# Kernel tuning notes

Measured on AMD Instinct MI355X. Metric: run time of the kernel, lower is better.

## Reference

```python
import jax, jax.numpy as jnp
import numpy as np

B, S, D, H, DH = 4, 2048, 1024, 16, 64
INIT_STD = 0.02
IGNORE = -100000.0


def setup_inputs() -> dict:
    key = jax.random.key(0)
    ks = jax.random.split(key, 5)
    x = jax.random.normal(ks[0], (B, S, D), dtype=jnp.float32)
    W_Q = INIT_STD * jax.random.normal(ks[1], (H, D, DH), dtype=jnp.float32)
    W_K = INIT_STD * jax.random.normal(ks[2], (H, D, DH), dtype=jnp.float32)
    W_V = INIT_STD * jax.random.normal(ks[3], (H, D, DH), dtype=jnp.float32)
    W_O = INIT_STD * jax.random.normal(ks[4], (H, DH, D), dtype=jnp.float32)
    b_Q = jnp.zeros((H, DH), dtype=jnp.float32)
    b_K = jnp.zeros((H, DH), dtype=jnp.float32)
    b_V = jnp.zeros((H, DH), dtype=jnp.float32)
    b_O = jnp.zeros((D,), dtype=jnp.float32)
    return {"x": x, "W_Q": W_Q, "b_Q": b_Q, "W_K": W_K, "b_K": b_K,
            "W_V": W_V, "b_V": b_V, "W_O": W_O, "b_O": b_O}


def reference(x, W_Q, b_Q, W_K, b_K, W_V, b_V, W_O, b_O):
    # x: (B, S, D); projections -> (B, S, H, DH)
    Q = jnp.einsum('bqd,hde->bqhe', x, W_Q) + b_Q
    K = jnp.einsum('bkd,hde->bkhe', x, W_K) + b_K
    V = jnp.einsum('bkd,hde->bkhe', x, W_V) + b_V
    d_head = Q.shape[-1]
    # scores: (B, H, Sq, Sk)
    scores = jnp.einsum('bqhe,bkhe->bhqk', Q, K) / np.sqrt(d_head).astype(np.float32)
    s = scores.shape[-1]
    causal = jnp.triu(jnp.ones((s, s), dtype=bool), k=1)
    scores = jnp.where(causal, jnp.float32(IGNORE), scores)
    A = jax.nn.softmax(scores, axis=-1)
    z = jnp.einsum('bhqk,bkhe->bqhe', A, V)
    # output projection: sum over heads + bias
    attn_out = jnp.einsum('bqhe,hed->bqd', z, W_O) + b_O
    return attn_out
```

## Files before the change

kernel.cpp:

```cpp
#include <hip/hip_runtime.h>


#define B_ 4
#define S_ 2048
#define D_ 1024
#define H_ 16
#define DH_ 64

typedef unsigned short ushort_t;
typedef __attribute__((ext_vector_type(4))) short short4v;
typedef __attribute__((ext_vector_type(8))) short short8v;
typedef __attribute__((ext_vector_type(4))) float floatx4;
typedef __attribute__((ext_vector_type(4))) unsigned short ushort4v;

static __device__ __forceinline__ ushort_t f2bf(float f) {
    union { float f; unsigned u; } v; v.f = f;
    unsigned r = v.u + 0x7fffu + ((v.u >> 16) & 1u);
    return (ushort_t)(r >> 16);
}

static __device__ __forceinline__ float fast_exp2(float x) {
#if __has_builtin(__builtin_amdgcn_exp2f)
    return __builtin_amdgcn_exp2f(x);
#else
    return exp2f(x);
#endif
}

static __device__ __forceinline__ unsigned pack_bf16_tr(float lo, float hi) {
    union { float f; unsigned u; } a, b;
    a.f = lo; b.f = hi;
    return __builtin_amdgcn_perm(b.u, a.u, 0x07060302u);
}

static __device__ __forceinline__ void g2lds16(const void* g, void* l) {
    __builtin_amdgcn_global_load_lds(
        (__attribute__((address_space(1))) void*)(unsigned long long)(size_t)g,
        (__attribute__((address_space(3))) void*)(unsigned int)(size_t)l,
        16, 0, 0);
}

__global__ void prep_kernel(const float* __restrict__ x,
                            const float* __restrict__ wq, const float* __restrict__ wk,
                            const float* __restrict__ wv, const float* __restrict__ wo,
                            ushort_t* __restrict__ xb, ushort_t* __restrict__ wt,
                            ushort_t* __restrict__ wot) {
    __shared__ float tile[32][33];
    int bid = blockIdx.x;
    int tid = threadIdx.x;
    if (bid < 8192) {
        int i = (bid * 256 + tid) * 4;
        float4 v = *(const float4*)&x[i];
        ushort4v o;
        o[0] = f2bf(v.x); o[1] = f2bf(v.y); o[2] = f2bf(v.z); o[3] = f2bf(v.w);
        *(ushort4v*)&xb[i] = o;
        return;
    }
    const float* src;
    ushort_t* d;
    int C, r0, c0;
    if (bid < 11264) {
        int t = bid - 8192;
        int z = t / 64, r = t % 64;
        src = (z < 16 ? wq : (z < 32 ? wk : wv)) + (size_t)(z & 15) * 65536;
        d = wt + (size_t)z * 65536;
        C = 64; r0 = (r >> 1) * 32; c0 = (r & 1) * 32;
    } else {
        int t = bid - 11264;
        int z = t / 64, r = t % 64;
        src = wo + (size_t)z * 65536;
        d = wot + (size_t)z * 64;
        C = 1024; r0 = (r & 1) * 32; c0 = (r >> 1) * 32;
    }
    int tx = tid & 31, ty = tid >> 5;
#pragma unroll
    for (int i = 0; i < 4; ++i)
        tile[ty + i * 8][tx] = src[(size_t)(r0 + ty + i * 8) * C + c0 + tx];
    __syncthreads();
#pragma unroll
    for (int i = 0; i < 4; ++i)
        d[(size_t)(c0 + ty + i * 8) * 1024 + r0 + tx] = f2bf(tile[tx][ty + i * 8]);
}


#define GQ_BAR() __builtin_amdgcn_s_barrier()
#define GQ_VM4 do { asm volatile("s_waitcnt vmcnt(4)"); __builtin_amdgcn_sched_barrier(0); } while (0)
#define GQ_VM2 do { asm volatile("s_waitcnt vmcnt(2)"); __builtin_amdgcn_sched_barrier(0); } while (0)
#define GQ_VM0 do { asm volatile("s_waitcnt vmcnt(0)"); __builtin_amdgcn_sched_barrier(0); } while (0)
#define GQ_WAITLG do { asm volatile("s_waitcnt lgkmcnt(0)"); __builtin_amdgcn_sched_barrier(0); } while (0)

#define GQ_READS_B(KB)                                                          \
    _Pragma("unroll") for (int nt = 0; nt < 4; ++nt)                            \
        bfr[KB][nt] = *(const short8v*)&cB[(wn * 64 + nt * 16) * 64 + ((KB) ? kb1 : kb0)];

#define GQ_READS_A(MH, KB)                                                      \
    _Pragma("unroll") for (int i = 0; i < 4; ++i)                               \
        af[i] = *(const short8v*)&cA[(wm * 128 + ((MH) * 4 + i) * 16) * 64 + ((KB) ? kb1 : kb0)];

#define GQ_MFMA(MH, KB)                                                         \
    GQ_WAITLG;                                                                  \
    __builtin_amdgcn_s_setprio(1);                                              \
    _Pragma("unroll") for (int i = 0; i < 4; ++i)                               \
        _Pragma("unroll") for (int nt = 0; nt < 4; ++nt)                        \
            acc[(MH) * 4 + i][nt] = __builtin_amdgcn_mfma_f32_16x16x32_bf16(    \
                af[i], bfr[KB][nt], acc[(MH) * 4 + i][nt], 0, 0, 0);            \
    __builtin_amdgcn_s_setprio(0);                                              \
    __builtin_amdgcn_sched_barrier(0);

#define GQ_KSTEP(CA, CB, S1, S2, S3, S4, WMID, WEND) do {                       \
    const ushort_t* cA = (CA); const ushort_t* cB = (CB);                       \
    short8v af[4]; short8v bfr[2][4];                                           \
    GQ_READS_B(0) GQ_READS_A(0, 0) S1; GQ_BAR();                                \
    GQ_MFMA(0, 0) GQ_BAR();                                                     \
    GQ_READS_B(1) GQ_READS_A(0, 1) S2; GQ_BAR();                                \
    GQ_MFMA(0, 1) WMID; GQ_BAR();                                               \
    GQ_READS_A(1, 0) S3; GQ_BAR();                                              \
    GQ_MFMA(1, 0) GQ_BAR();                                                     \
    GQ_READS_A(1, 1) S4; GQ_BAR();                                              \
    GQ_MFMA(1, 1) WEND; GQ_BAR();                                               \
} while (0)

__global__ __launch_bounds__(512, 2) void gemm_qkv(const ushort_t* __restrict__ A,
                                                   const ushort_t* __restrict__ Wt,
                                                   const float* __restrict__ bq,
                                                   const float* __restrict__ bk,
                                                   const float* __restrict__ bv,
                                                   ushort_t* __restrict__ Qw,
                                                   ushort_t* __restrict__ Kw,
                                                   ushort_t* __restrict__ Vw) {
    __shared__ ushort_t sA[2][256 * 64];
    __shared__ ushort_t sB[2][256 * 64];
    const int tid = threadIdx.x;
    const int lane = tid & 63, w = tid >> 6;
    const int lq = lane & 15, quad = lane >> 4;
    const int wm = w >> 2, wn = w & 3;
    const int m0 = blockIdx.x * 256, n0 = blockIdx.y * 256;

    const int kb0 = lq * 64 + ((quad ^ (lq & 7)) << 3);
    const int kb1 = lq * 64 + (((4 | quad) ^ (lq & 7)) << 3);

    const int uR = ((w & 4) << 5) + (w & 3) * 16;

    auto stageA2 = [&](ushort_t* dst, int kk, int R0) __attribute__((always_inline)) {
#pragma unroll
        for (int j = 0; j < 2; ++j) {
            int rr = R0 + j * 8 + (lane >> 3);
            int cc = (lane & 7) ^ (rr & 7);
            g2lds16(&A[(size_t)(m0 + rr) * 1024 + kk + cc * 8], &dst[(R0 + j * 8) * 64]);
        }
    };
    auto stageB2 = [&](ushort_t* dst, int kk, int R0) __attribute__((always_inline)) {
#pragma unroll
        for (int j = 0; j < 2; ++j) {
            int rr = R0 + j * 8 + (lane >> 3);
            int cc = (lane & 7) ^ (rr & 7);
            g2lds16(&Wt[(size_t)(n0 + rr) * 1024 + kk + cc * 8], &dst[(R0 + j * 8) * 64]);
        }
    };

    floatx4 acc[8][4] = {};

    stageA2(sA[0], 0, uR);
    stageB2(sB[0], 0, w * 32);
    stageB2(sB[0], 0, w * 32 + 16);
    stageA2(sA[0], 0, uR + 64);
    GQ_VM2;
    GQ_BAR();

    int p = 0;
    for (int t = 0; t < 15; ++t) {
        const int kk = (t + 1) * 64;
        ushort_t* nA = sA[p ^ 1];
        ushort_t* nB = sB[p ^ 1];
        GQ_KSTEP(sA[p], sB[p],
                 stageA2(nA, kk, uR),
                 stageB2(nB, kk, w * 32),
                 stageB2(nB, kk, w * 32 + 16),
                 stageA2(nA, kk, uR + 64),
                 GQ_VM4, GQ_VM2);
        p ^= 1;
    }
    GQ_KSTEP(sA[1], sB[1], (void)0, (void)0, (void)0, (void)0, GQ_VM0, (void)0);

    const int mat = blockIdx.y >> 2;
    const float* bias = mat == 0 ? bq : (mat == 1 ? bk : bv);
    const int colbase = (blockIdx.y & 3) * 256 + wn * 64;
    float bias_v[4];
#pragma unroll
    for (int nt = 0; nt < 4; ++nt) bias_v[nt] = bias[colbase + nt * 16 + lq];

#pragma unroll
    for (int mt = 0; mt < 8; ++mt) {
#pragma unroll
        for (int nt = 0; nt < 4; ++nt) {
            int row0 = m0 + wm * 128 + mt * 16 + quad * 4;
            int col = colbase + nt * 16 + lq;
            int h = col >> 6, e = col & 63;
            if (mat == 2) {
                int b = row0 >> 11, s = row0 & 2047;
                ushort4v pk;
#pragma unroll
                for (int rg = 0; rg < 4; ++rg) pk[rg] = f2bf(acc[mt][nt][rg] + bias_v[nt]);
                *(ushort4v*)&Vw[((size_t)((b << 4) | h) * 64 + e) * 2048 + s] = pk;
            } else {
                ushort_t* Du = mat == 0 ? Qw : Kw;
#pragma unroll
                for (int rg = 0; rg < 4; ++rg) {
                    int row = row0 + rg;
                    int b = row >> 11, s = row & 2047;
                    float v = acc[mt][nt][rg] + bias_v[nt];
                    if (mat == 0) v *= 0.18033688011112042f;
                    Du[((size_t)((b << 4) | h) * 2048 + s) * 64 + e] = f2bf(v);
                }
            }
        }
    }
}

#define VROW 140
__global__ __launch_bounds__(256) void attn_kernel(const ushort_t* __restrict__ Q,
                                                   const ushort_t* __restrict__ Kg,
                                                   const ushort_t* __restrict__ Vt,
                                                   ushort_t* __restrict__ Z) {
    __shared__ ushort_t sK[2][128 * 64];
    __shared__ ushort_t sV[64 * VROW];
    const int tid = threadIdx.x;
    const int lane = tid & 63, w = tid >> 6;
    const int lq = lane & 15, quad = lane >> 4;
    const int bh = blockIdx.x;
    const int b = bh >> 4, h = bh & 15;
    const ushort_t* Qp = Q + (size_t)bh * S_ * DH_;
    const ushort_t* Kp = Kg + (size_t)bh * S_ * DH_;
    const ushort_t* Vp = Vt + (size_t)bh * DH_ * S_;

    const int kbase0 = lq * 64 + ((quad ^ (lq & 7)) << 3);
    const int kbase1 = lq * 64 + (((4 | quad) ^ (lq & 7)) << 3);
    const int vbase = lq * VROW + quad * 4;
    const int vr = w * 16 + (lane >> 2);
    const int vc = (lane & 3) * 32;

    const floatx4 fzero = {0.f, 0.f, 0.f, 0.f};

    auto stageK = [&](int kt, int bs) __attribute__((always_inline)) {
        ushort_t* dK = sK[bs];
#pragma unroll
        for (int p = 0; p < 4; ++p) {
            int rrk = w * 32 + p * 8 + (lane >> 3);
            int ck = (lane & 7) ^ (rrk & 7);
            g2lds16(&Kp[(size_t)(kt * 128 + rrk) * 64 + ck * 8], &dK[(w * 32 + p * 8) * 64]);
        }
    };
    auto loadV = [&](int kt, short8v* vr4) __attribute__((always_inline)) {
        const ushort_t* src = &Vp[(size_t)vr * 2048 + kt * 128 + vc];
#pragma unroll
        for (int j = 0; j < 4; ++j) vr4[j] = *(const short8v*)&src[j * 8];
    };
    auto writeV = [&](const short8v* vr4) __attribute__((always_inline)) {
        ushort_t* dst = &sV[vr * VROW + vc];
#pragma unroll
        for (int j = 0; j < 4; ++j) *(short8v*)&dst[j * 8] = vr4[j];
    };

    for (int pass = 0; pass < 2; ++pass) {
        const int qt = pass == 0 ? (int)blockIdx.y : 15 - (int)blockIdx.y;
        const int q0 = qt * 128;

        short8v qf[2][2];
#pragma unroll
        for (int qi = 0; qi < 2; ++qi)
#pragma unroll
            for (int ks = 0; ks < 2; ++ks)
                qf[qi][ks] = *(const short8v*)&Qp[(size_t)(q0 + w * 32 + qi * 16 + lq) * DH_ + ks * 32 + quad * 8];

        float l_i[2] = {0.f, 0.f};
        floatx4 o[2][4] = {};
        short8v vreg[4];

        stageK(0, 0);
        loadV(0, vreg);

        for (int kt = 0; kt <= qt; ++kt) {
            const bool diag = (kt == qt);
            const ushort_t* cK = sK[kt & 1];

            __syncthreads();
            writeV(vreg);
            if (kt < qt) {
                stageK(kt + 1, (kt + 1) & 1);
                loadV(kt + 1, vreg);
            }

            floatx4 st[8][2];
#pragma unroll
            for (int si = 0; si < 8; ++si) {
                short8v a0 = *(const short8v*)&cK[kbase0 + si * 1024];
                short8v a1 = *(const short8v*)&cK[kbase1 + si * 1024];
#pragma unroll
                for (int qi = 0; qi < 2; ++qi) {
                    st[si][qi] = __builtin_amdgcn_mfma_f32_16x16x32_bf16(a0, qf[qi][0], fzero, 0, 0, 0);
                    st[si][qi] = __builtin_amdgcn_mfma_f32_16x16x32_bf16(a1, qf[qi][1], st[si][qi], 0, 0, 0);
                }
            }

            short4v pf[8][2];
#pragma unroll
            for (int qi = 0; qi < 2; ++qi) {
                const int qg = q0 + w * 32 + qi * 16 + lq;
                float lsum = 0.f;
#pragma unroll
                for (int si = 0; si < 8; ++si) {
                    float p[4];
#pragma unroll
                    for (int rg = 0; rg < 4; ++rg) {
                        float v = st[si][qi][rg];
                        if (diag) {
                            int sg = kt * 128 + si * 16 + quad * 4 + rg;
                            if (sg > qg) v = -1e30f;
                        }
                        p[rg] = fast_exp2(v);
                        lsum += p[rg];
                    }
                    union { unsigned u[2]; short4v v4; } pk;
                    pk.u[0] = pack_bf16_tr(p[0], p[1]);
                    pk.u[1] = pack_bf16_tr(p[2], p[3]);
                    pf[si][qi] = pk.v4;
                }
                l_i[qi] += lsum;
            }

            __syncthreads();

#pragma unroll
            for (int ksp = 0; ksp < 8; ++ksp) {
#pragma unroll
                for (int et = 0; et < 4; ++et) {
                    short4v vf = *(const short4v*)&sV[vbase + et * (16 * VROW) + ksp * 16];
#pragma unroll
                    for (int qi = 0; qi < 2; ++qi)
                        o[qi][et] = __builtin_amdgcn_mfma_f32_16x16x16bf16_1k(pf[ksp][qi], vf, o[qi][et], 0, 0, 0);
                }
            }
        }

#pragma unroll
        for (int qi = 0; qi < 2; ++qi) {
            float lf = l_i[qi];
            lf += __shfl_xor(lf, 16);
            lf += __shfl_xor(lf, 32);
            float linv[4];
#pragma unroll
            for (int rg = 0; rg < 4; ++rg) linv[rg] = 1.0f / __shfl(lf, quad * 4 + rg);
#pragma unroll
            for (int et = 0; et < 4; ++et) {
#pragma unroll
                for (int rg = 0; rg < 4; ++rg) {
                    int qg = q0 + w * 32 + qi * 16 + quad * 4 + rg;
                    int e = et * 16 + lq;
                    Z[((size_t)(b * S_ + qg) * H_ + h) * DH_ + e] = f2bf(o[qi][et][rg] * linv[rg]);
                }
            }
        }
    }
}

__global__ __launch_bounds__(256) void gemm_o(const ushort_t* __restrict__ A,
                                              const ushort_t* __restrict__ Bt,
                                              const float* __restrict__ bias,
                                              float* __restrict__ Dst) {
    __shared__ ushort_t sA[128 * 64];
    __shared__ ushort_t sB[128 * 64];
    const int tid = threadIdx.x;
    const int lane = tid & 63, w = tid >> 6;
    const int lq = lane & 15, quad = lane >> 4;
    const int wm = w >> 1, wn = w & 1;
    const int m0 = blockIdx.x * 128, n0 = blockIdx.y * 128;

    floatx4 acc[4][4] = {};

    for (int k0 = 0; k0 < 1024; k0 += 64) {
        __syncthreads();
#pragma unroll
        for (int p = 0; p < 4; ++p) {
            int rr = w * 32 + p * 8 + (lane >> 3);
            int cc = (lane & 7) ^ (rr & 7);
            g2lds16(&A[(size_t)(m0 + rr) * 1024 + k0 + cc * 8], &sA[(w * 32 + p * 8) * 64]);
            g2lds16(&Bt[(size_t)(n0 + rr) * 1024 + k0 + cc * 8], &sB[(w * 32 + p * 8) * 64]);
        }
        __syncthreads();
#pragma unroll
        for (int ks = 0; ks < 2; ++ks) {
            short8v af[4], bfr[4];
#pragma unroll
            for (int t = 0; t < 4; ++t) {
                int ma = wm * 64 + t * 16 + lq;
                af[t] = *(const short8v*)&sA[ma * 64 + ((((ks << 2) | quad) ^ (ma & 7)) << 3)];
                int nb = wn * 64 + t * 16 + lq;
                bfr[t] = *(const short8v*)&sB[nb * 64 + ((((ks << 2) | quad) ^ (nb & 7)) << 3)];
            }
#pragma unroll
            for (int mt = 0; mt < 4; ++mt)
#pragma unroll
                for (int nt = 0; nt < 4; ++nt)
                    acc[mt][nt] = __builtin_amdgcn_mfma_f32_16x16x32_bf16(af[mt], bfr[nt], acc[mt][nt], 0, 0, 0);
        }
    }

    float bias_v[4];
#pragma unroll
    for (int nt = 0; nt < 4; ++nt) bias_v[nt] = bias[n0 + wn * 64 + nt * 16 + lq];

#pragma unroll
    for (int mt = 0; mt < 4; ++mt) {
#pragma unroll
        for (int nt = 0; nt < 4; ++nt) {
            int row0 = m0 + wm * 64 + mt * 16 + quad * 4;
            int col = n0 + wn * 64 + nt * 16 + lq;
#pragma unroll
            for (int rg = 0; rg < 4; ++rg)
                Dst[(size_t)(row0 + rg) * 1024 + col] = acc[mt][nt][rg] + bias_v[nt];
        }
    }
}

extern "C" void kernel_launch(void* const* d_in, const int* in_sizes, int n_in,
                              void* d_out, int out_size, void* d_ws, size_t ws_size,
                              hipStream_t stream) {
    const float* x  = (const float*)d_in[0];
    const float* wq = (const float*)d_in[1];
    const float* bq = (const float*)d_in[2];
    const float* wk = (const float*)d_in[3];
    const float* bk = (const float*)d_in[4];
    const float* wv = (const float*)d_in[5];
    const float* bv = (const float*)d_in[6];
    const float* wo = (const float*)d_in[7];
    const float* bo = (const float*)d_in[8];

    char* ws = (char*)d_ws;
    size_t off = 0;
    ushort_t* xb  = (ushort_t*)(ws + off); off += (size_t)8192 * 1024 * 2;
    ushort_t* wt  = (ushort_t*)(ws + off); off += (size_t)3 * 1024 * 1024 * 2;
    ushort_t* wot = (ushort_t*)(ws + off); off += (size_t)1024 * 1024 * 2;
    ushort_t* Qw  = (ushort_t*)(ws + off); off += (size_t)8192 * 1024 * 2;
    ushort_t* Kw  = (ushort_t*)(ws + off); off += (size_t)8192 * 1024 * 2;
    ushort_t* Vw  = (ushort_t*)(ws + off); off += (size_t)8192 * 1024 * 2;
    ushort_t* Zw  = (ushort_t*)(ws + off); off += (size_t)8192 * 1024 * 2;

    prep_kernel<<<12288, 256, 0, stream>>>(x, wq, wk, wv, wo, xb, wt, wot);
    gemm_qkv<<<dim3(32, 12), 512, 0, stream>>>(xb, wt, bq, bk, bv, Qw, Kw, Vw);
    attn_kernel<<<dim3(64, 8), 256, 0, stream>>>(Qw, Kw, Vw, Zw);
    gemm_o<<<dim3(64, 8), 256, 0, stream>>>(Zw, wot, bo, (float*)d_out);
}
```

Baseline: 254.8 us.

## Shrink QKV GEMM tile to 128 rows and raise MFMA priority in attention

The QKV projection GEMM now uses a 128x256 output tile instead of 256x256, which doubles the grid to 768 blocks and halves the A-tile shared memory and accumulator registers. The load staging, wait counts and epilogue row mapping are reworked to fit. The aim is better fill of the GPU's many compute units with more, smaller blocks, at the cost of more B-matrix reloads per output. The attention kernel also wraps its QK and PV MFMA loops in s_setprio to favour the matrix-issuing waves.

Measured after the change: 262.6 us. +3.1%, slower.

```diff
diff --git a/kernel.cpp b/kernel.cpp
--- a/kernel.cpp
+++ b/kernel.cpp
@@ -85,7 +85,7 @@
 
 #define GQ_BAR() __builtin_amdgcn_s_barrier()
 #define GQ_VM4 do { asm volatile("s_waitcnt vmcnt(4)"); __builtin_amdgcn_sched_barrier(0); } while (0)
-#define GQ_VM2 do { asm volatile("s_waitcnt vmcnt(2)"); __builtin_amdgcn_sched_barrier(0); } while (0)
+#define GQ_VM1 do { asm volatile("s_waitcnt vmcnt(1)"); __builtin_amdgcn_sched_barrier(0); } while (0)
 #define GQ_VM0 do { asm volatile("s_waitcnt vmcnt(0)"); __builtin_amdgcn_sched_barrier(0); } while (0)
 #define GQ_WAITLG do { asm volatile("s_waitcnt lgkmcnt(0)"); __builtin_amdgcn_sched_barrier(0); } while (0)
 
@@ -94,22 +94,22 @@
         bfr[KB][nt] = *(const short8v*)&cB[(wn * 64 + nt * 16) * 64 + ((KB) ? kb1 : kb0)];
 
 #define GQ_READS_A(MH, KB)                                                      \
-    _Pragma("unroll") for (int i = 0; i < 4; ++i)                               \
-        af[i] = *(const short8v*)&cA[(wm * 128 + ((MH) * 4 + i) * 16) * 64 + ((KB) ? kb1 : kb0)];
+    _Pragma("unroll") for (int i = 0; i < 2; ++i)                               \
+        af[i] = *(const short8v*)&cA[(wm * 64 + ((MH) * 2 + i) * 16) * 64 + ((KB) ? kb1 : kb0)];
 
 #define GQ_MFMA(MH, KB)                                                         \
     GQ_WAITLG;                                                                  \
     __builtin_amdgcn_s_setprio(1);                                              \
-    _Pragma("unroll") for (int i = 0; i < 4; ++i)                               \
+    _Pragma("unroll") for (int i = 0; i < 2; ++i)                               \
         _Pragma("unroll") for (int nt = 0; nt < 4; ++nt)                        \
-            acc[(MH) * 4 + i][nt] = __builtin_amdgcn_mfma_f32_16x16x32_bf16(    \
-                af[i], bfr[KB][nt], acc[(MH) * 4 + i][nt], 0, 0, 0);            \
+            acc[(MH) * 2 + i][nt] = __builtin_amdgcn_mfma_f32_16x16x32_bf16(    \
+                af[i], bfr[KB][nt], acc[(MH) * 2 + i][nt], 0, 0, 0);            \
     __builtin_amdgcn_s_setprio(0);                                              \
     __builtin_amdgcn_sched_barrier(0);
 
 #define GQ_KSTEP(CA, CB, S1, S2, S3, S4, WMID, WEND) do {                       \
     const ushort_t* cA = (CA); const ushort_t* cB = (CB);                       \
-    short8v af[4]; short8v bfr[2][4];                                           \
+    short8v af[2]; short8v bfr[2][4];                                           \
     GQ_READS_B(0) GQ_READS_A(0, 0) S1; GQ_BAR();                                \
     GQ_MFMA(0, 0) GQ_BAR();                                                     \
     GQ_READS_B(1) GQ_READS_A(0, 1) S2; GQ_BAR();                                \
@@ -128,43 +128,39 @@
                                                    ushort_t* __restrict__ Qw,
                                                    ushort_t* __restrict__ Kw,
                                                    ushort_t* __restrict__ Vw) {
-    __shared__ ushort_t sA[2][256 * 64];
+    __shared__ ushort_t sA[2][128 * 64];
     __shared__ ushort_t sB[2][256 * 64];
     const int tid = threadIdx.x;
     const int lane = tid & 63, w = tid >> 6;
     const int lq = lane & 15, quad = lane >> 4;
     const int wm = w >> 2, wn = w & 3;
-    const int m0 = blockIdx.x * 256, n0 = blockIdx.y * 256;
+    const int m0 = blockIdx.x * 128, n0 = blockIdx.y * 256;
 
     const int kb0 = lq * 64 + ((quad ^ (lq & 7)) << 3);
     const int kb1 = lq * 64 + (((4 | quad) ^ (lq & 7)) << 3);
 
-    const int uR = ((w & 4) << 5) + (w & 3) * 16;
-
-    auto stageA2 = [&](ushort_t* dst, int kk, int R0) __attribute__((always_inline)) {
-#pragma unroll
-        for (int j = 0; j < 2; ++j) {
-            int rr = R0 + j * 8 + (lane >> 3);
-            int cc = (lane & 7) ^ (rr & 7);
-            g2lds16(&A[(size_t)(m0 + rr) * 1024 + kk + cc * 8], &dst[(R0 + j * 8) * 64]);
-        }
+    const int uRA = ((w >> 2) << 6) + (w & 3) * 8;
+
+    auto stageA1 = [&](ushort_t* dst, int kk, int R0) __attribute__((always_inline)) {
+        int rr = R0 + (lane >> 3);
+        int cc = (lane & 7) ^ (rr & 7);
+        g2lds16(&A[(size_t)(m0 + rr) * 1024 + kk + cc * 8], &dst[R0 * 64]);
     };
-    auto stageB2 = [&](ushort_t* dst, int kk, int R0) __attribute__((always_inline)) {
-#pragma unroll
-        for (int j = 0; j < 2; ++j) {
-            int rr = R0 + j * 8 + (lane >> 3);
-            int cc = (lane & 7) ^ (rr & 7);
-            g2lds16(&Wt[(size_t)(n0 + rr) * 1024 + kk + cc * 8], &dst[(R0 + j * 8) * 64]);
-        }
+    auto stageB1 = [&](ushort_t* dst, int kk, int R0) __attribute__((always_inline)) {
+        int rr = R0 + (lane >> 3);
+        int cc = (lane & 7) ^ (rr & 7);
+        g2lds16(&Wt[(size_t)(n0 + rr) * 1024 + kk + cc * 8], &dst[R0 * 64]);
     };
 
-    floatx4 acc[8][4] = {};
-
-    stageA2(sA[0], 0, uR);
-    stageB2(sB[0], 0, w * 32);
-    stageB2(sB[0], 0, w * 32 + 16);
-    stageA2(sA[0], 0, uR + 64);
-    GQ_VM2;
+    floatx4 acc[4][4] = {};
+
+    stageA1(sA[0], 0, uRA);
+    stageB1(sB[0], 0, w * 32);
+    stageB1(sB[0], 0, w * 32 + 8);
+    stageB1(sB[0], 0, w * 32 + 16);
+    stageB1(sB[0], 0, w * 32 + 24);
+    stageA1(sA[0], 0, uRA + 32);
+    GQ_VM1;
     GQ_BAR();
 
     int p = 0;
@@ -173,11 +169,11 @@
         ushort_t* nA = sA[p ^ 1];
         ushort_t* nB = sB[p ^ 1];
         GQ_KSTEP(sA[p], sB[p],
-                 stageA2(nA, kk, uR),
-                 stageB2(nB, kk, w * 32),
-                 stageB2(nB, kk, w * 32 + 16),
-                 stageA2(nA, kk, uR + 64),
-                 GQ_VM4, GQ_VM2);
+                 { stageA1(nA, kk, uRA); stageB1(nB, kk, w * 32); },
+                 { stageB1(nB, kk, w * 32 + 8); stageB1(nB, kk, w * 32 + 16); },
+                 { stageB1(nB, kk, w * 32 + 24); },
+                 { stageA1(nA, kk, uRA + 32); },
+                 GQ_VM4, GQ_VM1);
         p ^= 1;
     }
     GQ_KSTEP(sA[1], sB[1], (void)0, (void)0, (void)0, (void)0, GQ_VM0, (void)0);
@@ -190,10 +186,10 @@
     for (int nt = 0; nt < 4; ++nt) bias_v[nt] = bias[colbase + nt * 16 + lq];
 
 #pragma unroll
-    for (int mt = 0; mt < 8; ++mt) {
+    for (int mt = 0; mt < 4; ++mt) {
 #pragma unroll
         for (int nt = 0; nt < 4; ++nt) {
-            int row0 = m0 + wm * 128 + mt * 16 + quad * 4;
+            int row0 = m0 + wm * 64 + mt * 16 + quad * 4;
             int col = colbase + nt * 16 + lq;
             int h = col >> 6, e = col & 63;
             if (mat == 2) {
@@ -291,6 +287,7 @@
             }
 
             floatx4 st[8][2];
+            __builtin_amdgcn_s_setprio(1);
 #pragma unroll
             for (int si = 0; si < 8; ++si) {
                 short8v a0 = *(const short8v*)&cK[kbase0 + si * 1024];
@@ -301,6 +298,7 @@
                     st[si][qi] = __builtin_amdgcn_mfma_f32_16x16x32_bf16(a1, qf[qi][1], st[si][qi], 0, 0, 0);
                 }
             }
+            __builtin_amdgcn_s_setprio(0);
 
             short4v pf[8][2];
 #pragma unroll
@@ -330,6 +328,7 @@
 
             __syncthreads();
 
+            __builtin_amdgcn_s_setprio(1);
 #pragma unroll
             for (int ksp = 0; ksp < 8; ++ksp) {
 #pragma unroll
@@ -340,6 +339,7 @@
                         o[qi][et] = __builtin_amdgcn_mfma_f32_16x16x16bf16_1k(pf[ksp][qi], vf, o[qi][et], 0, 0, 0);
                 }
             }
+            __builtin_amdgcn_s_setprio(0);
         }
 
 #pragma unroll
@@ -446,7 +446,7 @@
     ushort_t* Zw  = (ushort_t*)(ws + off); off += (size_t)8192 * 1024 * 2;
 
     prep_kernel<<<12288, 256, 0, stream>>>(x, wq, wk, wv, wo, xb, wt, wot);
-    gemm_qkv<<<dim3(32, 12), 512, 0, stream>>>(xb, wt, bq, bk, bv, Qw, Kw, Vw);
+    gemm_qkv<<<dim3(64, 12), 512, 0, stream>>>(xb, wt, bq, bk, bv, Qw, Kw, Vw);
     attn_kernel<<<dim3(64, 8), 256, 0, stream>>>(Qw, Kw, Vw, Zw);
     gemm_o<<<dim3(64, 8), 256, 0, stream>>>(Zw, wot, bo, (float*)d_out);
 }
```
